# Kernel tuning notes

Hardware: AMD Instinct MI355X
Metric: run time of the kernel (lower is better)

Reference implementation:

```python
import jax, jax.numpy as jnp
import numpy as np

NUM_USERS = 200000
NUM_ITEMS = 100000
NUM_NODES = NUM_USERS + NUM_ITEMS
NUM_EDGES = 600000
DIM = 128
BATCH = 16384


def setup_inputs() -> dict:
    key = jax.random.key(0)
    ks = jax.random.split(key, 7)
    return {
        "user_indices": jax.random.randint(ks[0], (BATCH,), 0, NUM_USERS),
        "item_indices": jax.random.randint(ks[1], (BATCH,), 0, NUM_ITEMS),
        "user_emb": jax.random.normal(ks[2], (NUM_USERS, DIM), jnp.float32) * 0.01,
        "item_emb": jax.random.normal(ks[3], (NUM_ITEMS, DIM), jnp.float32) * 0.01,
        "W": jax.random.normal(ks[4], (DIM, DIM), jnp.float32) * (1.0 / np.sqrt(DIM)),
        "b": jax.random.normal(ks[5], (DIM,), jnp.float32) * 0.01,
        "edge_index": jax.random.randint(ks[6], (2, NUM_EDGES), 0, NUM_NODES),
    }


def reference(user_indices, item_indices, user_emb, item_emb, W, b, edge_index):
    # all node features: [N, D]
    nodes = jnp.concatenate([user_emb, item_emb], axis=0)
    src, dst = edge_index[0], edge_index[1]
    # gather neighbor features [E, D], scatter-add into [N, D]
    agg = jax.ops.segment_sum(nodes[src], dst, num_segments=NUM_NODES)
    # linear transform (nn.Linear: x @ W.T + b)
    prop = agg @ W.T + b
    u = prop[:NUM_USERS][user_indices]   # [B, D]
    i = prop[NUM_USERS:][item_indices]   # [B, D]
    return jnp.sum(u * i, axis=1, keepdims=True)  # [B, 1]
```

## Files before the change

### kernel.cpp

```cpp
#include <hip/hip_runtime.h>

#define NUM_USERS 200000
#define NUM_ITEMS 100000
#define NUM_NODES 300000
#define NUM_EDGES 600000
#define DIM      128
#define BATCH    16384
#define NSLOTS   (2 * BATCH)
#define CAP      32

typedef __attribute__((ext_vector_type(4))) float f32x4;
typedef __attribute__((ext_vector_type(8))) short bf16x8;

static __device__ __forceinline__ ushort f2bf(float x) {
    unsigned u = __float_as_uint(x);
    return (ushort)((u + 0x7FFF + ((u >> 16) & 1)) >> 16);
}

__global__ void wconv(const float* __restrict__ W, ushort* __restrict__ Wb) {
    int t = blockIdx.x * 256 + threadIdx.x;
    float4 v = ((const float4*)W)[t];
    ushort4 o = { f2bf(v.x), f2bf(v.y), f2bf(v.z), f2bf(v.w) };
    ((ushort4*)Wb)[t] = o;
}

__global__ void build_map(const int* __restrict__ uidx, const int* __restrict__ iidx,
                          int* __restrict__ map) {
    int t = blockIdx.x * 256 + threadIdx.x;
    if (t >= NSLOTS) return;
    int node = (t < BATCH) ? uidx[t] : (NUM_USERS + iidx[t - BATCH]);
    atomicCAS(&map[node], -1, t);
}

__global__ void bin_edges(const int* __restrict__ edges, const int* __restrict__ map,
                          int* __restrict__ cnt, int* __restrict__ bucket) {
    int e = blockIdx.x * 256 + threadIdx.x;
    if (e >= NUM_EDGES) return;
    int dst = edges[NUM_EDGES + e];
    int s = map[dst];
    if (s < 0) return;
    int src = edges[e];
    int p = atomicAdd(&cnt[s], 1);
    if (p < CAP) bucket[s * CAP + p] = src;
}

__global__ __launch_bounds__(256) void gather(const int* __restrict__ cnt,
                                              const int* __restrict__ bucket,
                                              const float* __restrict__ uemb,
                                              const float* __restrict__ iemb,
                                              ushort* __restrict__ aggb) {
    int s = blockIdx.x * 4 + (threadIdx.x >> 6);
    int lane = threadIdx.x & 63;
    int n = cnt[s]; if (n > CAP) n = CAP;
    const int* bk = bucket + s * CAP;

    float2 v[4];
#pragma unroll
    for (int k = 0; k < 4; ++k) {
        int src = bk[k];
        if (src < 0 || src >= NUM_NODES) src = 0;
        const float* row = (src < NUM_USERS)
            ? uemb + (size_t)src * DIM
            : iemb + (size_t)(src - NUM_USERS) * DIM;
        v[k] = ((const float2*)row)[lane];
    }
    float2 acc = {0.f, 0.f};
#pragma unroll
    for (int k = 0; k < 4; ++k)
        if (k < n) { acc.x += v[k].x; acc.y += v[k].y; }
    for (int k = 4; k < n; ++k) {
        int src = bk[k];
        const float* row = (src < NUM_USERS)
            ? uemb + (size_t)src * DIM
            : iemb + (size_t)(src - NUM_USERS) * DIM;
        float2 t = ((const float2*)row)[lane];
        acc.x += t.x; acc.y += t.y;
    }
    ushort2 ob = { f2bf(acc.x), f2bf(acc.y) };
    ((ushort2*)(aggb + (size_t)s * DIM))[lane] = ob;
}

__global__ __launch_bounds__(256) void transform_mfma(
        const ushort* __restrict__ aggb, const ushort* __restrict__ Wb,
        const float* __restrict__ bias, float* __restrict__ prop) {
    int wave = threadIdx.x >> 6, lane = threadIdx.x & 63;
    int lr = lane & 15, lg = lane >> 4;
    int s0 = blockIdx.x * 64 + wave * 16;

    f32x4 acc[8];
#pragma unroll
    for (int jt = 0; jt < 8; ++jt) acc[jt] = (f32x4){0.f, 0.f, 0.f, 0.f};

    const ushort* pa = aggb + (size_t)(s0 + lr) * DIM + lg * 8;
    const ushort* pw = Wb + lr * DIM + lg * 8;
#pragma unroll
    for (int ks = 0; ks < 4; ++ks) {
        bf16x8 af = *(const bf16x8*)(pa + ks * 32);
#pragma unroll
        for (int jt = 0; jt < 8; ++jt) {
            bf16x8 wf = *(const bf16x8*)(pw + jt * 16 * DIM + ks * 32);
            acc[jt] = __builtin_amdgcn_mfma_f32_16x16x32_bf16(af, wf, acc[jt], 0, 0, 0);
        }
    }
#pragma unroll
    for (int jt = 0; jt < 8; ++jt) {
        float bj = bias[jt * 16 + lr];
#pragma unroll
        for (int r = 0; r < 4; ++r)
            prop[(size_t)(s0 + lg * 4 + r) * DIM + jt * 16 + lr] = acc[jt][r] + bj;
    }
}

__global__ void final_dot(const int* __restrict__ uidx, const int* __restrict__ iidx,
                          const int* __restrict__ map, const float* __restrict__ prop,
                          float* __restrict__ out) {
    int o = blockIdx.x * 4 + (threadIdx.x >> 6);
    if (o >= BATCH) return;
    int lane = threadIdx.x & 63;
    int su = map[uidx[o]];
    int si = map[NUM_USERS + iidx[o]];
    float2 a = ((const float2*)(prop + (size_t)su * DIM))[lane];
    float2 c = ((const float2*)(prop + (size_t)si * DIM))[lane];
    float v = a.x * c.x + a.y * c.y;
#pragma unroll
    for (int off = 32; off > 0; off >>= 1) v += __shfl_down(v, off);
    if (lane == 0) out[o] = v;
}

extern "C" void kernel_launch(void* const* d_in, const int* in_sizes, int n_in,
                              void* d_out, int out_size, void* d_ws, size_t ws_size,
                              hipStream_t stream) {
    const int*   uidx  = (const int*)d_in[0];
    const int*   iidx  = (const int*)d_in[1];
    const float* uemb  = (const float*)d_in[2];
    const float* iemb  = (const float*)d_in[3];
    const float* W     = (const float*)d_in[4];
    const float* bias  = (const float*)d_in[5];
    const int*   edges = (const int*)d_in[6];
    float*       out   = (float*)d_out;

    char* ws = (char*)d_ws;
    int*    map    = (int*)ws;
    int*    cnt    = (int*)(ws + (2u << 20));
    int*    bucket = (int*)(ws + (3u << 20));
    ushort* Wb     = (ushort*)(ws + (7u << 20));
    ushort* aggb   = (ushort*)(ws + (8u << 20));
    float*  prop   = (float*)(ws + (16u << 20));

    hipMemsetAsync(map, 0xFF, NUM_NODES * sizeof(int), stream);
    hipMemsetAsync(cnt, 0, NSLOTS * sizeof(int), stream);

    wconv<<<16, 256, 0, stream>>>(W, Wb);
    build_map<<<(NSLOTS + 255) / 256, 256, 0, stream>>>(uidx, iidx, map);
    bin_edges<<<(NUM_EDGES + 255) / 256, 256, 0, stream>>>(edges, map, cnt, bucket);
    gather<<<NSLOTS / 4, 256, 0, stream>>>(cnt, bucket, uemb, iemb, aggb);
    transform_mfma<<<NSLOTS / 64, 256, 0, stream>>>(aggb, Wb, bias, prop);
    final_dot<<<(BATCH + 3) / 4, 256, 0, stream>>>(uidx, iidx, map, prop, out);
}
```

Baseline: 213.8 us.

## Fuse setup kernels, split transform across waves by column, store prop as bf16

```diff
diff --git a/kernel.cpp b/kernel.cpp
--- a/kernel.cpp
+++ b/kernel.cpp
@@ -16,20 +16,27 @@
     unsigned u = __float_as_uint(x);
     return (ushort)((u + 0x7FFF + ((u >> 16) & 1)) >> 16);
 }
-
-__global__ void wconv(const float* __restrict__ W, ushort* __restrict__ Wb) {
-    int t = blockIdx.x * 256 + threadIdx.x;
-    float4 v = ((const float4*)W)[t];
-    ushort4 o = { f2bf(v.x), f2bf(v.y), f2bf(v.z), f2bf(v.w) };
-    ((ushort4*)Wb)[t] = o;
+static __device__ __forceinline__ float bf2f(ushort x) {
+    return __uint_as_float(((unsigned)x) << 16);
 }
 
-__global__ void build_map(const int* __restrict__ uidx, const int* __restrict__ iidx,
-                          int* __restrict__ map) {
-    int t = blockIdx.x * 256 + threadIdx.x;
-    if (t >= NSLOTS) return;
-    int node = (t < BATCH) ? uidx[t] : (NUM_USERS + iidx[t - BATCH]);
-    atomicCAS(&map[node], -1, t);
+__global__ __launch_bounds__(256) void init_misc(const float* __restrict__ W,
+                                                 ushort* __restrict__ Wb,
+                                                 const int* __restrict__ uidx,
+                                                 const int* __restrict__ iidx,
+                                                 int* __restrict__ map) {
+    int b = blockIdx.x;
+    if (b < 16) {
+        int t = b * 256 + threadIdx.x;
+        float4 v = ((const float4*)W)[t];
+        ushort4 o = { f2bf(v.x), f2bf(v.y), f2bf(v.z), f2bf(v.w) };
+        ((ushort4*)Wb)[t] = o;
+    } else {
+        int t = (b - 16) * 256 + threadIdx.x;
+        if (t >= NSLOTS) return;
+        int node = (t < BATCH) ? uidx[t] : (NUM_USERS + iidx[t - BATCH]);
+        atomicCAS(&map[node], -1, t);
+    }
 }
 
 __global__ void bin_edges(const int* __restrict__ edges, const int* __restrict__ map,
@@ -82,46 +89,45 @@
 
 __global__ __launch_bounds__(256) void transform_mfma(
         const ushort* __restrict__ aggb, const ushort* __restrict__ Wb,
-        const float* __restrict__ bias, float* __restrict__ prop) {
-    int wave = threadIdx.x >> 6, lane = threadIdx.x & 63;
+        const float* __restrict__ bias, ushort* __restrict__ propb) {
+    int gw = blockIdx.x * 4 + (threadIdx.x >> 6);
+    int lane = threadIdx.x & 63;
+    int stile = gw >> 2;
+    int jq = gw & 3;
     int lr = lane & 15, lg = lane >> 4;
-    int s0 = blockIdx.x * 64 + wave * 16;
+    int s0 = stile * 16;
 
-    f32x4 acc[8];
-#pragma unroll
-    for (int jt = 0; jt < 8; ++jt) acc[jt] = (f32x4){0.f, 0.f, 0.f, 0.f};
-
+    f32x4 acc0 = {0.f, 0.f, 0.f, 0.f}, acc1 = {0.f, 0.f, 0.f, 0.f};
     const ushort* pa = aggb + (size_t)(s0 + lr) * DIM + lg * 8;
-    const ushort* pw = Wb + lr * DIM + lg * 8;
+    const ushort* pw = Wb + (size_t)(jq * 32 + lr) * DIM + lg * 8;
 #pragma unroll
     for (int ks = 0; ks < 4; ++ks) {
         bf16x8 af = *(const bf16x8*)(pa + ks * 32);
+        bf16x8 w0 = *(const bf16x8*)(pw + ks * 32);
+        bf16x8 w1 = *(const bf16x8*)(pw + 16 * DIM + ks * 32);
+        acc0 = __builtin_amdgcn_mfma_f32_16x16x32_bf16(af, w0, acc0, 0, 0, 0);
+        acc1 = __builtin_amdgcn_mfma_f32_16x16x32_bf16(af, w1, acc1, 0, 0, 0);
+    }
+    float b0 = bias[jq * 32 + lr], b1 = bias[jq * 32 + 16 + lr];
 #pragma unroll
-        for (int jt = 0; jt < 8; ++jt) {
-            bf16x8 wf = *(const bf16x8*)(pw + jt * 16 * DIM + ks * 32);
-            acc[jt] = __builtin_amdgcn_mfma_f32_16x16x32_bf16(af, wf, acc[jt], 0, 0, 0);
-        }
-    }
-#pragma unroll
-    for (int jt = 0; jt < 8; ++jt) {
-        float bj = bias[jt * 16 + lr];
-#pragma unroll
-        for (int r = 0; r < 4; ++r)
-            prop[(size_t)(s0 + lg * 4 + r) * DIM + jt * 16 + lr] = acc[jt][r] + bj;
+    for (int r = 0; r < 4; ++r) {
+        size_t row = (size_t)(s0 + lg * 4 + r) * DIM;
+        propb[row + jq * 32 + lr]      = f2bf(acc0[r] + b0);
+        propb[row + jq * 32 + 16 + lr] = f2bf(acc1[r] + b1);
     }
 }
 
 __global__ void final_dot(const int* __restrict__ uidx, const int* __restrict__ iidx,
-                          const int* __restrict__ map, const float* __restrict__ prop,
+                          const int* __restrict__ map, const ushort* __restrict__ propb,
                           float* __restrict__ out) {
     int o = blockIdx.x * 4 + (threadIdx.x >> 6);
     if (o >= BATCH) return;
     int lane = threadIdx.x & 63;
     int su = map[uidx[o]];
     int si = map[NUM_USERS + iidx[o]];
-    float2 a = ((const float2*)(prop + (size_t)su * DIM))[lane];
-    float2 c = ((const float2*)(prop + (size_t)si * DIM))[lane];
-    float v = a.x * c.x + a.y * c.y;
+    ushort2 a = ((const ushort2*)(propb + (size_t)su * DIM))[lane];
+    ushort2 c = ((const ushort2*)(propb + (size_t)si * DIM))[lane];
+    float v = bf2f(a.x) * bf2f(c.x) + bf2f(a.y) * bf2f(c.y);
 #pragma unroll
     for (int off = 32; off > 0; off >>= 1) v += __shfl_down(v, off);
     if (lane == 0) out[o] = v;
@@ -145,15 +151,14 @@
     int*    bucket = (int*)(ws + (3u << 20));
     ushort* Wb     = (ushort*)(ws + (7u << 20));
     ushort* aggb   = (ushort*)(ws + (8u << 20));
-    float*  prop   = (float*)(ws + (16u << 20));
+    ushort* propb  = (ushort*)(ws + (16u << 20));
 
     hipMemsetAsync(map, 0xFF, NUM_NODES * sizeof(int), stream);
     hipMemsetAsync(cnt, 0, NSLOTS * sizeof(int), stream);
 
-    wconv<<<16, 256, 0, stream>>>(W, Wb);
-    build_map<<<(NSLOTS + 255) / 256, 256, 0, stream>>>(uidx, iidx, map);
+    init_misc<<<16 + (NSLOTS + 255) / 256, 256, 0, stream>>>(W, Wb, uidx, iidx, map);
     bin_edges<<<(NUM_EDGES + 255) / 256, 256, 0, stream>>>(edges, map, cnt, bucket);
     gather<<<NSLOTS / 4, 256, 0, stream>>>(cnt, bucket, uemb, iemb, aggb);
-    transform_mfma<<<NSLOTS / 64, 256, 0, stream>>>(aggb, Wb, bias, prop);
-    final_dot<<<(BATCH + 3) / 4, 256, 0, stream>>>(uidx, iidx, map, prop, out);
+    transform_mfma<<<NSLOTS / 16, 256, 0, stream>>>(aggb, Wb, bias, propb);
+    final_dot<<<(BATCH + 3) / 4, 256, 0, stream>>>(uidx, iidx, map, propb, out);
 }
```

Result: no change. 210.9 us (-1.4%).
